# Performance work log

Hardware: AMD Instinct MI355X
Metric: run time of the kernel (lower is better)

Reference implementation:

```python
import jax, jax.numpy as jnp
import numpy as np

N_NODES = 100000
N_EDGES = 800000
F_IN = 128
F_OUT = 128
K_HOPS = 2


def setup_inputs() -> dict:
    key = jax.random.key(0)
    k1, k2, k3 = jax.random.split(key, 3)
    x = jax.random.normal(k1, (N_NODES, F_IN), dtype=jnp.float32)
    edge_index = jax.random.randint(k2, (2, N_EDGES), 0, N_NODES, dtype=jnp.int64)
    # SGConv's internal Linear(num_features -> embedding_size), bias=True
    W = jax.random.normal(k3, (F_OUT, F_IN), dtype=jnp.float32) * (1.0 / np.sqrt(F_IN))
    b = jnp.zeros((F_OUT,), dtype=jnp.float32)
    return {"x": x, "W": W, "b": b, "edge_index": edge_index}


def reference(x, W, b, edge_index):
    N = x.shape[0]
    # gcn_norm: add self loops (weight 1), symmetric normalization D^-1/2 (A+I) D^-1/2
    loop = jnp.arange(N, dtype=edge_index.dtype)
    row = jnp.concatenate([edge_index[0], loop])  # source nodes j
    col = jnp.concatenate([edge_index[1], loop])  # target nodes i
    ones = jnp.ones(row.shape[0], dtype=x.dtype)
    deg = jax.ops.segment_sum(ones, col, num_segments=N)
    dinv = jnp.where(deg > 0, jax.lax.rsqrt(deg), jnp.zeros_like(deg))
    norm = dinv[row] * dinv[col]  # [E+N]
    # K-hop propagation: x <- segment_sum(norm * x[row] -> col)
    h = x
    for _ in range(K_HOPS):
        h = jax.ops.segment_sum(norm[:, None] * h[row], col, num_segments=N)
    out = h @ W.T + b  # [N, F_OUT]
    return jax.nn.log_softmax(out, axis=1)
```

## Files before the change

kernel.cpp:

```cpp
#include <hip/hip_runtime.h>
#include <math.h>

#define N_NODES 100000
#define N_EDGES 800000
#define F 128
#define NBUCK ((N_NODES + 255) / 256)
#define CPAD 32
#define SCAP 3072
#define BSPAN 4096
#define EPB 2048
#define FILL_BLOCKS ((N_EDGES + EPB - 1) / EPB)

typedef __attribute__((ext_vector_type(8))) short short8;
typedef __attribute__((ext_vector_type(4))) float floatx4;

__device__ __forceinline__ unsigned short f2bf(float f) {
    unsigned u = __float_as_uint(f);
    u += 0x7fffu + ((u >> 16) & 1u);
    return (unsigned short)(u >> 16);
}
__device__ __forceinline__ float bf_lo(unsigned u) { return __uint_as_float(u << 16); }
__device__ __forceinline__ float bf_hi(unsigned u) { return __uint_as_float(u & 0xffff0000u); }
__device__ __forceinline__ unsigned pack2(float a, float b) {
    return (unsigned)f2bf(a) | ((unsigned)f2bf(b) << 16);
}


__global__ __launch_bounds__(256) void k_fill3(const int* __restrict__ row,
                                               const int* __restrict__ col,
                                               int* __restrict__ bcnt,
                                               unsigned* __restrict__ stage) {
    __shared__ int hist[512];
    __shared__ int base[512];
    __shared__ int gpos[NBUCK];
    __shared__ int sA[256], sB[256];
    __shared__ unsigned buf[EPB];
    __shared__ unsigned short bkt[EPB];
    int t = threadIdx.x, blk = blockIdx.x;
    int e0 = blk * EPB;
    int nedge = N_EDGES - e0; if (nedge > EPB) nedge = EPB;

    hist[t] = 0; hist[256 + t] = 0;
    __syncthreads();

    int myb[8]; unsigned myv[8];
#pragma unroll
    for (int k = 0; k < 8; ++k) {
        int i = t + k * 256;
        myb[k] = -1;
        if (i < nedge) {
            int e = e0 + i;
            int r = row[e], c = col[e];
            int bk = c >> 8;
            myb[k] = bk;
            myv[k] = ((unsigned)(c & 255) << 20) | (unsigned)(r + 1);
            atomicAdd(&hist[bk], 1);
        }
    }
    __syncthreads();

    int v0 = hist[t], v1 = hist[256 + t];
    sA[t] = v0; __syncthreads();
#pragma unroll
    for (int off = 1; off < 256; off <<= 1) {
        int u = (t >= off) ? sA[t - off] : 0;
        __syncthreads(); sA[t] += u; __syncthreads();
    }
    int tot0 = sA[255];
    sB[t] = v1; __syncthreads();
#pragma unroll
    for (int off = 1; off < 256; off <<= 1) {
        int u = (t >= off) ? sB[t - off] : 0;
        __syncthreads(); sB[t] += u; __syncthreads();
    }
    base[t] = sA[t] - v0;
    base[256 + t] = tot0 + sB[t] - v1;
    __syncthreads();
    hist[t] = base[t]; hist[256 + t] = base[256 + t];
    __syncthreads();

#pragma unroll
    for (int k = 0; k < 8; ++k) {
        if (myb[k] >= 0) {
            int pos = atomicAdd(&hist[myb[k]], 1);
            buf[pos] = myv[k];
            bkt[pos] = (unsigned short)myb[k];
        }
    }
    __syncthreads();

    for (int i = t; i < NBUCK; i += 256) {
        int cnt = hist[i] - base[i];
        gpos[i] = cnt > 0 ? atomicAdd(&bcnt[i * CPAD], cnt) : 0;
    }
    __syncthreads();

    for (int i = t; i < nedge; i += 256) {
        int bk = bkt[i];
        int op = gpos[bk] + (i - base[bk]);
        if (op < SCAP)
            stage[(size_t)bk * SCAP + op] = buf[i];
    }
}


__global__ __launch_bounds__(256) void k_build(const int* __restrict__ bcnt,
                                               const unsigned* __restrict__ stage,
                                               unsigned* __restrict__ csr,
                                               int2* __restrict__ rp2,
                                               float* __restrict__ dinv,
                                               float* __restrict__ dinv2) {
    __shared__ int hist[256];
    __shared__ int sc[256];
    __shared__ int cursor[256];
    __shared__ int spanTot;
    __shared__ unsigned img[BSPAN];
    int bk = blockIdx.x, t = threadIdx.x;
    int n = bcnt[bk * CPAD]; n = n < SCAP ? n : SCAP;
    const unsigned* sp = stage + (size_t)bk * SCAP;
    hist[t] = 0;
    __syncthreads();
    for (int i = t; i < n; i += 256) atomicAdd(&hist[sp[i] >> 20], 1);
    __syncthreads();
    int cdeg = hist[t];
    int pad = (cdeg + 7) & ~7;
    sc[t] = pad;
    __syncthreads();
#pragma unroll
    for (int off = 1; off < 256; off <<= 1) {
        int u = (t >= off) ? sc[t - off] : 0;
        __syncthreads();
        sc[t] += u;
        __syncthreads();
    }
    int excl = sc[t] - pad;
    if (t == 255) spanTot = sc[255];
    cursor[t] = excl;
    __syncthreads();
    int tot = spanTot;
    int node = bk * 256 + t;
    if (node < N_NODES) {
        int base = bk * BSPAN;
        rp2[node] = (int2){base + excl, base + excl + pad};
        float d = rsqrtf((float)cdeg + 1.0f);
        dinv[node] = d; dinv2[node] = d * d;
    }
    for (int i = t; i < tot; i += 256) img[i] = 0u;
    __syncthreads();
    for (int i = t; i < n; i += 256) {
        unsigned v = sp[i];
        int pos = atomicAdd(&cursor[v >> 20], 1);
        img[pos] = v & 0xFFFFFu;
    }
    __syncthreads();
    unsigned* op = csr + (size_t)bk * BSPAN;
    for (int i = t; i < tot; i += 256) op[i] = img[i];
}

__global__ void k_prep(const float4* __restrict__ x, const float* __restrict__ dinv,
                       const float4* __restrict__ W4, uint2* __restrict__ wbf,
                       uint2* __restrict__ xb, uint2* __restrict__ h1b) {
    int i = blockIdx.x * blockDim.x + threadIdx.x;
    if (i < 32) { xb[i] = (uint2){0u, 0u}; h1b[i] = (uint2){0u, 0u}; }
    if (i < 4096) {
        float4 wv = W4[i];
        uint2 o; o.x = pack2(wv.x, wv.y); o.y = pack2(wv.z, wv.w);
        wbf[i] = o;
    }
    if (i >= N_NODES * 32) return;
    int node = i >> 5;
    float d = dinv[node];
    float4 v = x[i];
    uint2 o; o.x = pack2(d * v.x, d * v.y); o.y = pack2(d * v.z, d * v.w);
    xb[i + 32] = o;
}


__global__ __launch_bounds__(256) void k_hop(const int2* __restrict__ rp2,
                                             const unsigned* __restrict__ csr,
                                             const float* __restrict__ scale,
                                             const uint2* __restrict__ src,
                                             uint2* __restrict__ dst) {
    int wv = (blockIdx.x * blockDim.x + threadIdx.x) >> 6;
    int lane = threadIdx.x & 63;
    int half = lane >> 5, off = lane & 31;
    int node = wv * 2 + half;
    if (node >= N_NODES) return;
    uint2 u = src[(size_t)(node + 1) * 32 + off];
    float a0 = bf_lo(u.x), a1 = bf_hi(u.x);
    float a2 = bf_lo(u.y), a3 = bf_hi(u.y);
    int2 rp = rp2[node];
    int e = rp.x, end = rp.y;
    for (; e < end; e += 8) {
        const uint4* cp = (const uint4*)(csr + e);
        uint4 c0 = cp[0], c1 = cp[1];
        unsigned idx[8] = {c0.x, c0.y, c0.z, c0.w, c1.x, c1.y, c1.z, c1.w};
#pragma unroll
        for (int j = 0; j < 8; ++j) {
            uint2 v = src[(size_t)idx[j] * 32 + off];
            a0 += bf_lo(v.x); a1 += bf_hi(v.x);
            a2 += bf_lo(v.y); a3 += bf_hi(v.y);
        }
    }
    float s = scale[node];
    uint2 o; o.x = pack2(s * a0, s * a1); o.y = pack2(s * a2, s * a3);
    dst[(size_t)(node + 1) * 32 + off] = o;
}


__global__ __launch_bounds__(256) void k_gemm_lsm_mfma(const unsigned short* __restrict__ h,
                                                       const unsigned short* __restrict__ wbf,
                                                       const float* __restrict__ b,
                                                       float* __restrict__ out) {
    int tid = threadIdx.x;
    int lane = tid & 63;
    int wave = tid >> 6;
    int m = lane & 15, quad = lane >> 4;

    float bv[8];
#pragma unroll
    for (int t = 0; t < 8; ++t) bv[t] = b[16 * t + m];

    const int ngroups = (N_NODES + 63) / 64;
    int g0 = blockIdx.x;
    short8 a[4];
    if (g0 < ngroups) {
        int nodeA = g0 * 64 + wave * 16 + m;
        int node_c = nodeA < N_NODES ? nodeA : N_NODES - 1;
#pragma unroll
        for (int ks = 0; ks < 4; ++ks)
            a[ks] = *(const short8*)(h + (size_t)node_c * 128 + ks * 32 + quad * 8);
    }
    for (int g = g0; g < ngroups; g += gridDim.x) {
        int gn = g + gridDim.x; if (gn >= ngroups) gn = g;
        int nodeN = gn * 64 + wave * 16 + m;
        int node_n = nodeN < N_NODES ? nodeN : N_NODES - 1;
        short8 an[4];
#pragma unroll
        for (int ks = 0; ks < 4; ++ks)
            an[ks] = *(const short8*)(h + (size_t)node_n * 128 + ks * 32 + quad * 8);

        int gbase = g * 64 + wave * 16;
        floatx4 acc[8];
#pragma unroll
        for (int t = 0; t < 8; ++t) acc[t] = (floatx4){bv[t], bv[t], bv[t], bv[t]};
#pragma unroll
        for (int t = 0; t < 8; ++t) {
#pragma unroll
            for (int ks = 0; ks < 4; ++ks) {
                short8 bf = *(const short8*)(wbf + (size_t)(16 * t + m) * 128 + ks * 32 + quad * 8);
                acc[t] = __builtin_amdgcn_mfma_f32_16x16x32_bf16(a[ks], bf, acc[t], 0, 0, 0);
            }
        }

#pragma unroll
        for (int r = 0; r < 4; ++r) {
            float mx = acc[0][r];
#pragma unroll
            for (int t = 1; t < 8; ++t) mx = fmaxf(mx, acc[t][r]);
#pragma unroll
            for (int msk = 1; msk < 16; msk <<= 1) mx = fmaxf(mx, __shfl_xor(mx, msk));
            float sm = 0.f;
#pragma unroll
            for (int t = 0; t < 8; ++t) sm += __expf(acc[t][r] - mx);
#pragma unroll
            for (int msk = 1; msk < 16; msk <<= 1) sm += __shfl_xor(sm, msk);
            float l = mx + __logf(sm);
            int rown = gbase + quad * 4 + r;
            if (rown < N_NODES) {
                float* op = out + (size_t)rown * 128 + m;
#pragma unroll
                for (int t = 0; t < 8; ++t) op[16 * t] = acc[t][r] - l;
            }
        }
#pragma unroll
        for (int ks = 0; ks < 4; ++ks) a[ks] = an[ks];
    }
}


extern "C" void kernel_launch(void* const* d_in, const int* in_sizes, int n_in,
                              void* d_out, int out_size, void* d_ws, size_t ws_size,
                              hipStream_t stream) {
    const float* x = (const float*)d_in[0];
    const float* W = (const float*)d_in[1];
    const float* b = (const float*)d_in[2];
    const int* edge = (const int*)d_in[3];
    const int* row = edge;
    const int* col = edge + N_EDGES;
    float* out = (float*)d_out;

    int*      bcnt  = (int*)d_ws;
    float*    dinv  = (float*)(bcnt + NBUCK * CPAD + 256);
    float*    dinv2 = dinv + 102400;
    int2*     rp2   = (int2*)(dinv2 + 102400);
    unsigned* csr   = (unsigned*)(rp2 + 102400);
    uint2*    xb    = (uint2*)(csr + (size_t)NBUCK * BSPAN);
    uint2*    h1b   = xb + 32 * (N_NODES + 1);
    uint2*    h2b   = xb;
    unsigned* stage = (unsigned*)(h1b + 32);
    uint2*    wbf   = h1b + 32 * (N_NODES + 1);

    int nb_prep = (N_NODES * 32 + 255) / 256;

    (void)hipMemsetAsync(bcnt, 0, (size_t)NBUCK * CPAD * 4, stream);
    k_fill3<<<FILL_BLOCKS, 256, 0, stream>>>(row, col, bcnt, stage);
    k_build<<<NBUCK, 256, 0, stream>>>(bcnt, stage, csr, rp2, dinv, dinv2);
    k_prep<<<nb_prep, 256, 0, stream>>>((const float4*)x, dinv, (const float4*)W, wbf, xb, h1b);

    int hop_blocks = (N_NODES / 2 * 64) / 256;
    k_hop<<<hop_blocks, 256, 0, stream>>>(rp2, csr, dinv2, xb, h1b);
    k_hop<<<hop_blocks, 256, 0, stream>>>(rp2, csr, dinv, h1b, h2b);

    k_gemm_lsm_mfma<<<512, 256, 0, stream>>>((const unsigned short*)(h2b + 32),
                                             (const unsigned short*)wbf, b, out);
}
```

Measured before the change: 219.5 us.

## Replace global-atomic bucket staging with per-block segments and fuse prep into build

k_fill3 no longer claims space with global atomics into per-bucket staging. Each block writes its locally bucket-sorted edges and its per-bucket base offsets to its own slot. k_build then reads every fill block's segment for its bucket to build the histogram and the CSR image. This removes the memset and the contended global atomics, and the separate k_prep kernel is folded in: weight conversion goes to fill block 0 and the scaling and bf16 conversion of x goes into k_build. The trade-off is that each build block now does short, scattered reads across all 391 fill segments, and threads walk those segments serially.

New measurement: 235.2 us. 7.1% more time.

```diff
diff --git a/kernel.cpp b/kernel.cpp
--- a/kernel.cpp
+++ b/kernel.cpp
@@ -5,11 +5,10 @@
 #define N_EDGES 800000
 #define F 128
 #define NBUCK ((N_NODES + 255) / 256)
-#define CPAD 32
-#define SCAP 3072
 #define BSPAN 4096
 #define EPB 2048
 #define FILL_BLOCKS ((N_EDGES + EPB - 1) / EPB)
+#define BSTRIDE 392
 
 typedef __attribute__((ext_vector_type(8))) short short8;
 typedef __attribute__((ext_vector_type(4))) float floatx4;
@@ -28,17 +27,28 @@
 
 __global__ __launch_bounds__(256) void k_fill3(const int* __restrict__ row,
                                                const int* __restrict__ col,
-                                               int* __restrict__ bcnt,
-                                               unsigned* __restrict__ stage) {
+                                               int* __restrict__ baseg,
+                                               unsigned* __restrict__ stage,
+                                               const float4* __restrict__ W4,
+                                               uint2* __restrict__ wbf,
+                                               uint2* __restrict__ xb,
+                                               uint2* __restrict__ h1b) {
     __shared__ int hist[512];
     __shared__ int base[512];
-    __shared__ int gpos[NBUCK];
     __shared__ int sA[256], sB[256];
     __shared__ unsigned buf[EPB];
-    __shared__ unsigned short bkt[EPB];
     int t = threadIdx.x, blk = blockIdx.x;
     int e0 = blk * EPB;
     int nedge = N_EDGES - e0; if (nedge > EPB) nedge = EPB;
+
+    if (blk == 0) {
+        for (int i = t; i < 4096; i += 256) {
+            float4 wv = W4[i];
+            uint2 o; o.x = pack2(wv.x, wv.y); o.y = pack2(wv.z, wv.w);
+            wbf[i] = o;
+        }
+        if (t < 32) { xb[t] = (uint2){0u, 0u}; h1b[t] = (uint2){0u, 0u}; }
+    }
 
     hist[t] = 0; hist[256 + t] = 0;
     __syncthreads();
@@ -84,43 +94,42 @@
         if (myb[k] >= 0) {
             int pos = atomicAdd(&hist[myb[k]], 1);
             buf[pos] = myv[k];
-            bkt[pos] = (unsigned short)myb[k];
-        }
-    }
-    __syncthreads();
-
-    for (int i = t; i < NBUCK; i += 256) {
-        int cnt = hist[i] - base[i];
-        gpos[i] = cnt > 0 ? atomicAdd(&bcnt[i * CPAD], cnt) : 0;
-    }
-    __syncthreads();
-
-    for (int i = t; i < nedge; i += 256) {
-        int bk = bkt[i];
-        int op = gpos[bk] + (i - base[bk]);
-        if (op < SCAP)
-            stage[(size_t)bk * SCAP + op] = buf[i];
-    }
-}
-
-
-__global__ __launch_bounds__(256) void k_build(const int* __restrict__ bcnt,
+        }
+    }
+    __syncthreads();
+
+    for (int i = t; i < BSTRIDE; i += 256) baseg[blk * BSTRIDE + i] = base[i];
+    for (int i = t; i < nedge; i += 256) stage[(size_t)blk * EPB + i] = buf[i];
+}
+
+
+__global__ __launch_bounds__(256) void k_build(const int* __restrict__ baseg,
                                                const unsigned* __restrict__ stage,
                                                unsigned* __restrict__ csr,
                                                int2* __restrict__ rp2,
                                                float* __restrict__ dinv,
-                                               float* __restrict__ dinv2) {
+                                               float* __restrict__ dinv2,
+                                               const float4* __restrict__ x4,
+                                               uint2* __restrict__ xb) {
     __shared__ int hist[256];
     __shared__ int sc[256];
     __shared__ int cursor[256];
+    __shared__ float dl[256];
+    __shared__ int rs[FILL_BLOCKS], re[FILL_BLOCKS];
     __shared__ int spanTot;
     __shared__ unsigned img[BSPAN];
     int bk = blockIdx.x, t = threadIdx.x;
-    int n = bcnt[bk * CPAD]; n = n < SCAP ? n : SCAP;
-    const unsigned* sp = stage + (size_t)bk * SCAP;
     hist[t] = 0;
-    __syncthreads();
-    for (int i = t; i < n; i += 256) atomicAdd(&hist[sp[i] >> 20], 1);
+    for (int blk = t; blk < FILL_BLOCKS; blk += 256) {
+        rs[blk] = baseg[blk * BSTRIDE + bk];
+        re[blk] = baseg[blk * BSTRIDE + bk + 1];
+    }
+    __syncthreads();
+    for (int blk = t; blk < FILL_BLOCKS; blk += 256) {
+        const unsigned* sp = stage + (size_t)blk * EPB;
+        for (int i = rs[blk]; i < re[blk]; ++i)
+            atomicAdd(&hist[sp[i] >> 20], 1);
+    }
     __syncthreads();
     int cdeg = hist[t];
     int pad = (cdeg + 7) & ~7;
@@ -136,43 +145,40 @@
     int excl = sc[t] - pad;
     if (t == 255) spanTot = sc[255];
     cursor[t] = excl;
-    __syncthreads();
-    int tot = spanTot;
+    float d = rsqrtf((float)cdeg + 1.0f);
+    dl[t] = d;
+    __syncthreads();
+    int tot = spanTot < BSPAN ? spanTot : BSPAN;
     int node = bk * 256 + t;
     if (node < N_NODES) {
         int base = bk * BSPAN;
         rp2[node] = (int2){base + excl, base + excl + pad};
-        float d = rsqrtf((float)cdeg + 1.0f);
         dinv[node] = d; dinv2[node] = d * d;
     }
     for (int i = t; i < tot; i += 256) img[i] = 0u;
     __syncthreads();
-    for (int i = t; i < n; i += 256) {
-        unsigned v = sp[i];
-        int pos = atomicAdd(&cursor[v >> 20], 1);
-        img[pos] = v & 0xFFFFFu;
+    for (int blk = t; blk < FILL_BLOCKS; blk += 256) {
+        const unsigned* sp = stage + (size_t)blk * EPB;
+        for (int i = rs[blk]; i < re[blk]; ++i) {
+            unsigned v = sp[i];
+            int pos = atomicAdd(&cursor[v >> 20], 1);
+            if (pos < BSPAN) img[pos] = v & 0xFFFFFu;
+        }
     }
     __syncthreads();
     unsigned* op = csr + (size_t)bk * BSPAN;
     for (int i = t; i < tot; i += 256) op[i] = img[i];
-}
-
-__global__ void k_prep(const float4* __restrict__ x, const float* __restrict__ dinv,
-                       const float4* __restrict__ W4, uint2* __restrict__ wbf,
-                       uint2* __restrict__ xb, uint2* __restrict__ h1b) {
-    int i = blockIdx.x * blockDim.x + threadIdx.x;
-    if (i < 32) { xb[i] = (uint2){0u, 0u}; h1b[i] = (uint2){0u, 0u}; }
-    if (i < 4096) {
-        float4 wv = W4[i];
-        uint2 o; o.x = pack2(wv.x, wv.y); o.y = pack2(wv.z, wv.w);
-        wbf[i] = o;
-    }
-    if (i >= N_NODES * 32) return;
-    int node = i >> 5;
-    float d = dinv[node];
-    float4 v = x[i];
-    uint2 o; o.x = pack2(d * v.x, d * v.y); o.y = pack2(d * v.z, d * v.w);
-    xb[i + 32] = o;
+
+    for (int i = t; i < 256 * 32; i += 256) {
+        int ln = i >> 5;
+        int nd = bk * 256 + ln;
+        if (nd < N_NODES) {
+            float dd = dl[ln];
+            float4 v = x4[(size_t)nd * 32 + (i & 31)];
+            uint2 o; o.x = pack2(dd * v.x, dd * v.y); o.y = pack2(dd * v.z, dd * v.w);
+            xb[(size_t)(nd + 1) * 32 + (i & 31)] = o;
+        }
+    }
 }
 
 
@@ -290,8 +296,8 @@
     const int* col = edge + N_EDGES;
     float* out = (float*)d_out;
 
-    int*      bcnt  = (int*)d_ws;
-    float*    dinv  = (float*)(bcnt + NBUCK * CPAD + 256);
+    int*      baseg = (int*)d_ws;
+    float*    dinv  = (float*)(baseg + 153856);
     float*    dinv2 = dinv + 102400;
     int2*     rp2   = (int2*)(dinv2 + 102400);
     unsigned* csr   = (unsigned*)(rp2 + 102400);
@@ -301,12 +307,10 @@
     unsigned* stage = (unsigned*)(h1b + 32);
     uint2*    wbf   = h1b + 32 * (N_NODES + 1);
 
-    int nb_prep = (N_NODES * 32 + 255) / 256;
-
-    (void)hipMemsetAsync(bcnt, 0, (size_t)NBUCK * CPAD * 4, stream);
-    k_fill3<<<FILL_BLOCKS, 256, 0, stream>>>(row, col, bcnt, stage);
-    k_build<<<NBUCK, 256, 0, stream>>>(bcnt, stage, csr, rp2, dinv, dinv2);
-    k_prep<<<nb_prep, 256, 0, stream>>>((const float4*)x, dinv, (const float4*)W, wbf, xb, h1b);
+    k_fill3<<<FILL_BLOCKS, 256, 0, stream>>>(row, col, baseg, stage,
+                                             (const float4*)W, wbf, xb, h1b);
+    k_build<<<NBUCK, 256, 0, stream>>>(baseg, stage, csr, rp2, dinv, dinv2,
+                                       (const float4*)x, xb);
 
     int hop_blocks = (N_NODES / 2 * 64) / 256;
     k_hop<<<hop_blocks, 256, 0, stream>>>(rp2, csr, dinv2, xb, h1b);
```
